# Kernel optimization log

Hardware: AMD Instinct MI355X
Metric: run time of the kernel (lower is better)

## Reference

```python
import jax, jax.numpy as jnp
import numpy as np

NUM_NODES = 100000
EMBED_DIM = 128
HIDDEN_DIM = 128
NUM_EDGES = 600000
NUM_LABELS = 200000


def setup_inputs() -> dict:
    key = jax.random.key(0)
    ks = jax.random.split(key, 12)
    edge_index = jax.random.randint(ks[0], (2, NUM_EDGES), 0, NUM_NODES)
    edge_label_index = jax.random.randint(ks[1], (2, NUM_LABELS), 0, NUM_NODES)
    s = 0.05
    return {
        "edge_index": edge_index,
        "edge_label_index": edge_label_index,
        "emb": jax.random.normal(ks[2], (NUM_NODES, EMBED_DIM), jnp.float32) * s,
        # conv1: lin_l (aggregated neighbors, with bias), lin_r (root, no bias)
        "W1l": jax.random.normal(ks[3], (EMBED_DIM, HIDDEN_DIM), jnp.float32) * s,
        "b1": jnp.zeros((HIDDEN_DIM,), jnp.float32),
        "W1r": jax.random.normal(ks[4], (EMBED_DIM, HIDDEN_DIM), jnp.float32) * s,
        # conv2
        "W2l": jax.random.normal(ks[5], (HIDDEN_DIM, HIDDEN_DIM), jnp.float32) * s,
        "b2": jnp.zeros((HIDDEN_DIM,), jnp.float32),
        "W2r": jax.random.normal(ks[6], (HIDDEN_DIM, HIDDEN_DIM), jnp.float32) * s,
        # final link predictor Linear(2*hidden, 1)
        "Wlin": jax.random.normal(ks[7], (2 * HIDDEN_DIM, 1), jnp.float32) * s,
        "blin": jnp.zeros((1,), jnp.float32),
    }


def _sage_conv(x, src, dst, Wl, bl, Wr):
    # mean aggregation of source-node features at destination nodes
    n = x.shape[0]
    msg_sum = jax.ops.segment_sum(x[src], dst, num_segments=n)  # [N, d]
    cnt = jax.ops.segment_sum(jnp.ones_like(src, dtype=x.dtype), dst, num_segments=n)
    agg = msg_sum / jnp.maximum(cnt, 1.0)[:, None]
    return agg @ Wl + bl + x @ Wr


def reference(edge_index, edge_label_index, emb, W1l, b1, W1r, W2l, b2, W2r, Wlin, blin):
    src, dst = edge_index[0], edge_index[1]
    x = jax.nn.relu(_sage_conv(emb, src, dst, W1l, b1, W1r))
    x = _sage_conv(x, src, dst, W2l, b2, W2r)
    s, d = edge_label_index[0], edge_label_index[1]
    pair = jnp.concatenate([x[s], x[d]], axis=1)  # [L, 2*hidden]
    return (pair @ Wlin + blin).reshape(-1)
```

## Files before the change

kernel.cpp:

```cpp
#include <hip/hip_runtime.h>
#include <hip/hip_bf16.h>

#define N_NODES 100000
#define N_EDGES 600000
#define N_LABELS 200000
#define DIM 128
#define NPARTS 391
#define MT 64
#define NMT 1563
#define FG_GRID 768
#define LDA 136
#define LDC 280

using short8 = __attribute__((ext_vector_type(8))) short;
using f32x2  = __attribute__((ext_vector_type(2))) float;
using f32x4  = __attribute__((ext_vector_type(4))) float;
using u32x2  = __attribute__((ext_vector_type(2))) unsigned;
using u32x4  = __attribute__((ext_vector_type(4))) unsigned;

__device__ __forceinline__ float b2f(short s) {
    union { unsigned u; float f; } c;
    c.u = ((unsigned)(unsigned short)s) << 16;
    return c.f;
}
__device__ __forceinline__ f32x2 b2f2(unsigned u) {
    union { unsigned u; float f; } lo, hi;
    lo.u = u << 16;
    hi.u = u & 0xffff0000u;
    f32x2 r; r[0] = lo.f; r[1] = hi.f;
    return r;
}
__device__ __forceinline__ short f2b(float f) {
    __hip_bfloat16 h = __float2bfloat16(f);
    return *reinterpret_cast<short*>(&h);
}
__device__ __forceinline__ unsigned f2b2u(float x, float y) {
    __hip_bfloat162 h = __float22bfloat162_rn(make_float2(x, y));
    return *reinterpret_cast<unsigned*>(&h);
}

__global__ void prep_k(const float* __restrict__ W1l, const float* __restrict__ W1r,
                       short* __restrict__ BT1,
                       const float* __restrict__ W2l, const float* __restrict__ W2r,
                       const float* __restrict__ Wlin, const float* __restrict__ b2,
                       float* __restrict__ up, float* __restrict__ uq,
                       float* __restrict__ vp, float* __restrict__ vq,
                       float2* __restrict__ cpq, int* __restrict__ cnt) {
    int b = blockIdx.x;
    int t = threadIdx.x;
    if (b < 128) {
        int i = b * 256 + t;
        int n = i >> 7, k = i & 127;
        float v = (n < 128) ? W1l[k * 128 + n] : W1r[k * 128 + (n - 128)];
        BT1[n * 128 + k] = f2b(v);
    } else if (b == 128) {
        const float* W = (t < 128) ? W2l : W2r;
        int k = t & 127;
        float s0 = 0.f, s1 = 0.f;
        for (int n = 0; n < 128; ++n) {
            float w = W[k * 128 + n];
            s0 += w * Wlin[n];
            s1 += w * Wlin[128 + n];
        }
        if (t < 128) { up[k] = s0; uq[k] = s1; }
        else         { vp[k] = s0; vq[k] = s1; }
    } else if (b == 129) {
        if (t < 64) {
            float p0 = b2[t] * Wlin[t] + b2[t + 64] * Wlin[t + 64];
            float q0 = b2[t] * Wlin[128 + t] + b2[t + 64] * Wlin[192 + t];
#pragma unroll
            for (int m = 1; m <= 32; m <<= 1) {
                p0 += __shfl_xor(p0, m, 64);
                q0 += __shfl_xor(q0, m, 64);
            }
            if (t == 0) *cpq = make_float2(p0, q0);
        }
    } else {
        int i = (b - 130) * 256 + t;
        if (i < N_NODES) cnt[i] = 0;
    }
}

__global__ void count_k(const int* __restrict__ ei, int* __restrict__ cnt,
                        int* __restrict__ rank) {
    int e = blockIdx.x * blockDim.x + threadIdx.x;
    if (e < N_EDGES) rank[e] = atomicAdd(&cnt[ei[N_EDGES + e]], 1);
}

__global__ void scan1_k(const int* __restrict__ cnt, int* __restrict__ rowptr,
                        int* __restrict__ partials) {
    __shared__ int s[256];
    int t = threadIdx.x;
    int i = blockIdx.x * 256 + t;
    int v = (i < N_NODES) ? cnt[i] : 0;
    s[t] = v;
    __syncthreads();
    for (int off = 1; off < 256; off <<= 1) {
        int x = s[t];
        int y = (t >= off) ? s[t - off] : 0;
        __syncthreads();
        s[t] = x + y;
        __syncthreads();
    }
    if (i < N_NODES) rowptr[i] = s[t] - v;
    if (t == 255) partials[blockIdx.x] = s[255];
}

__global__ void scanB_k(const int* __restrict__ partials, int* __restrict__ rowptr) {
    __shared__ int s[512];
    __shared__ int base_s;
    int t = threadIdx.x;
    int v = (t < NPARTS) ? partials[t] : 0;
    s[t] = v;
    __syncthreads();
    for (int off = 1; off < 512; off <<= 1) {
        int x = s[t];
        int y = (t >= off) ? s[t - off] : 0;
        __syncthreads();
        s[t] = x + y;
        __syncthreads();
    }
    int b = blockIdx.x;
    if (t == 0) base_s = (b > 0) ? s[b - 1] : 0;
    if (b == 0 && t == 0) rowptr[N_NODES] = s[NPARTS - 1];
    __syncthreads();
    if (t < 256) {
        int i = b * 256 + t;
        if (i < N_NODES) rowptr[i] += base_s;
    }
}

__global__ __launch_bounds__(256, 3) void fillgemm_k(const int* __restrict__ ei,
                                                     const int* __restrict__ rank,
                                                     const int* __restrict__ rowptr,
                                                     int* __restrict__ adj,
                                                     const float* __restrict__ Af,
                                                     const short* __restrict__ BT,
                                                     short* __restrict__ Hl,
                                                     short* __restrict__ Hr) {
    __shared__ short lA[MT * LDA];
    __shared__ short lC[MT * LDC];
    int tid = threadIdx.x;

    for (int e = blockIdx.x * 256 + tid; e < N_EDGES; e += FG_GRID * 256) {
        int d = ei[N_EDGES + e];
        adj[rowptr[d] + rank[e]] = ei[e];
    }

    int lane = tid & 63;
    int wave = tid >> 6;
    int quad = lane >> 4;
    int l16  = lane & 15;

    short8 Wf[4][4];
#pragma unroll
    for (int t = 0; t < 4; ++t)
#pragma unroll
        for (int kk = 0; kk < 4; ++kk)
            Wf[t][kk] = *(const short8*)(BT + (wave * 64 + t * 16 + l16) * DIM + kk * 32 + quad * 8);

    for (int mt = blockIdx.x; mt < NMT; mt += FG_GRID) {
        long base = (long)mt * MT;

        __syncthreads();
#pragma unroll
        for (int i = 0; i < 8; ++i) {
            int c = tid + i * 256;
            int row = c >> 5;
            int k4 = (c & 31) << 2;
            long grow = base + row;
            f32x4 a;
            if (grow < N_NODES) a = *(const f32x4*)(Af + grow * DIM + k4);
            else { a[0] = 0.f; a[1] = 0.f; a[2] = 0.f; a[3] = 0.f; }
            u32x2 o;
            o[0] = f2b2u(a[0], a[1]);
            o[1] = f2b2u(a[2], a[3]);
            *(u32x2*)(lA + row * LDA + k4) = o;
        }
        __syncthreads();

#pragma unroll
        for (int sub = 0; sub < 4; ++sub) {
            int r0 = sub * 16;
            short8 xf[4];
#pragma unroll
            for (int kk = 0; kk < 4; ++kk)
                xf[kk] = *(const short8*)(lA + (r0 + l16) * LDA + kk * 32 + quad * 8);
            f32x4 acc[4];
#pragma unroll
            for (int t = 0; t < 4; ++t)
#pragma unroll
                for (int r = 0; r < 4; ++r) acc[t][r] = 0.f;
#pragma unroll
            for (int kk = 0; kk < 4; ++kk)
#pragma unroll
                for (int t = 0; t < 4; ++t)
                    acc[t] = __builtin_amdgcn_mfma_f32_16x16x32_bf16(Wf[t][kk], xf[kk], acc[t], 0, 0, 0);
#pragma unroll
            for (int t = 0; t < 4; ++t) {
                u32x2 o;
                o[0] = f2b2u(acc[t][0], acc[t][1]);
                o[1] = f2b2u(acc[t][2], acc[t][3]);
                *(u32x2*)(lC + (r0 + l16) * LDC + wave * 64 + t * 16 + quad * 4) = o;
            }
        }
        __syncthreads();

#pragma unroll
        for (int half = 0; half < 2; ++half) {
            short* __restrict__ H = half ? Hr : Hl;
#pragma unroll
            for (int i = 0; i < 4; ++i) {
                int c2 = tid + i * 256;
                int row = c2 >> 4;
                int f8 = (c2 & 15) << 3;
                long grow = base + row;
                if (grow < N_NODES) {
                    short8 v = *(const short8*)(lC + row * LDC + half * 128 + f8);
                    *(short8*)(H + grow * DIM + f8) = v;
                }
            }
        }
    }
}

__device__ __forceinline__ void gather_mean(const short* __restrict__ Hl,
                                            const int* __restrict__ rowptr,
                                            const int* __restrict__ adj,
                                            int node, int lane, f32x2 sum[4], float& inv) {
    int g  = lane >> 4;
    int f0 = (lane & 15) << 3;
    int beg = rowptr[node];
    int deg = rowptr[node + 1] - beg;
#pragma unroll
    for (int d = 0; d < 4; ++d) { sum[d][0] = 0.f; sum[d][1] = 0.f; }

    int av = (lane < deg) ? adj[beg + lane] : 0;
    int degc = deg < 64 ? deg : 64;

    u32x4 h0;
    bool v0 = false;
    if (degc > 0) {
        int idx = __shfl(av, g, 64);
        v0 = g < degc;
        if (v0) h0 = *(const u32x4*)(Hl + (long)idx * DIM + f0);
    }
    for (int e0 = 4; e0 < degc; e0 += 4) {
        int idx = __shfl(av, e0 + g, 64);
        bool v1 = (e0 + g) < degc;
        u32x4 h1;
        if (v1) h1 = *(const u32x4*)(Hl + (long)idx * DIM + f0);
        if (v0) {
#pragma unroll
            for (int d = 0; d < 4; ++d) sum[d] += b2f2(h0[d]);
        }
        h0 = h1; v0 = v1;
    }
    if (v0) {
#pragma unroll
        for (int d = 0; d < 4; ++d) sum[d] += b2f2(h0[d]);
    }
    for (int e0 = 64; e0 < deg; e0 += 4) {
        int e = e0 + g;
        if (e < deg) {
            int idx = adj[beg + e];
            u32x4 h = *(const u32x4*)(Hl + (long)idx * DIM + f0);
#pragma unroll
            for (int d = 0; d < 4; ++d) sum[d] += b2f2(h[d]);
        }
    }
#pragma unroll
    for (int d = 0; d < 4; ++d)
#pragma unroll
        for (int c = 0; c < 2; ++c) {
            sum[d][c] += __shfl_xor(sum[d][c], 16, 64);
            sum[d][c] += __shfl_xor(sum[d][c], 32, 64);
        }
    inv = deg > 0 ? 1.f / (float)deg : 0.f;
}

__global__ void agg1_k(const short* __restrict__ Hl, const short* __restrict__ Hr,
                       const int* __restrict__ rowptr, const int* __restrict__ adj,
                       const float* __restrict__ b1,
                       const float* __restrict__ up, const float* __restrict__ uq,
                       const float* __restrict__ vp, const float* __restrict__ vq,
                       float2* __restrict__ S, float2* __restrict__ T) {
    int lane = threadIdx.x & 63;
    int node = blockIdx.x * 4 + (threadIdx.x >> 6);
    int f0 = (lane & 15) << 3;
    if (node >= N_NODES) return;

    f32x2 sum[4]; float inv;
    gather_mean(Hl, rowptr, adj, node, lane, sum, inv);

    u32x4 hru = *(const u32x4*)(Hr + (long)node * DIM + f0);
    f32x2 x2[4];
#pragma unroll
    for (int d = 0; d < 4; ++d) {
        f32x2 hr2 = b2f2(hru[d]);
        f32x2 bb  = *(const f32x2*)(b1 + f0 + 2 * d);
        f32x2 v   = sum[d] * inv + hr2 + bb;
        x2[d][0] = fmaxf(v[0], 0.f);
        x2[d][1] = fmaxf(v[1], 0.f);
    }

    f32x2 ap2 = {0.f, 0.f}, aq2 = {0.f, 0.f}, tp2 = {0.f, 0.f}, tq2 = {0.f, 0.f};
#pragma unroll
    for (int d = 0; d < 4; ++d) {
        f32x2 u0 = *(const f32x2*)(up + f0 + 2 * d);
        f32x2 u1 = *(const f32x2*)(uq + f0 + 2 * d);
        f32x2 w0 = *(const f32x2*)(vp + f0 + 2 * d);
        f32x2 w1 = *(const f32x2*)(vq + f0 + 2 * d);
        ap2 += x2[d] * u0;
        aq2 += x2[d] * u1;
        tp2 += x2[d] * w0;
        tq2 += x2[d] * w1;
    }
    float ap = ap2[0] + ap2[1], aq = aq2[0] + aq2[1];
    float tp = tp2[0] + tp2[1], tq = tq2[0] + tq2[1];
#pragma unroll
    for (int m = 1; m <= 8; m <<= 1) {
        ap += __shfl_xor(ap, m, 64);
        aq += __shfl_xor(aq, m, 64);
        tp += __shfl_xor(tp, m, 64);
        tq += __shfl_xor(tq, m, 64);
    }
    if (lane == 0) {
        S[node] = make_float2(ap, aq);
        T[node] = make_float2(tp, tq);
    }
}

__global__ void agg2_k(const int* __restrict__ rowptr, const int* __restrict__ adj,
                       const float2* __restrict__ S, const float2* __restrict__ T,
                       const float2* __restrict__ cpq,
                       float* __restrict__ p, float* __restrict__ q) {
    int lane = threadIdx.x & 63;
    int wavei = blockIdx.x * 4 + (threadIdx.x >> 6);
    int slot = lane & 3;
    int node = wavei * 16 + (lane >> 2);
    if (node >= N_NODES) return;
    int beg = rowptr[node], end = rowptr[node + 1];
    float sp = 0.f, sq = 0.f;
    for (int e = beg + slot; e < end; e += 4) {
        float2 v = S[adj[e]];
        sp += v.x; sq += v.y;
    }
    sp += __shfl_xor(sp, 1, 64); sp += __shfl_xor(sp, 2, 64);
    sq += __shfl_xor(sq, 1, 64); sq += __shfl_xor(sq, 2, 64);
    if (slot == 0) {
        int deg = end - beg;
        float inv = deg > 0 ? 1.f / (float)deg : 0.f;
        float2 t = T[node];
        float2 c = *cpq;
        p[node] = sp * inv + t.x + c.x;
        q[node] = sq * inv + t.y + c.y;
    }
}

__global__ void out_k(const int* __restrict__ eli, const float* __restrict__ p,
                      const float* __restrict__ q, const float* __restrict__ blin,
                      float* __restrict__ out) {
    int i = blockIdx.x * blockDim.x + threadIdx.x;
    if (i < N_LABELS) out[i] = p[eli[i]] + q[eli[N_LABELS + i]] + blin[0];
}


extern "C" void kernel_launch(void* const* d_in, const int* in_sizes, int n_in,
                              void* d_out, int out_size, void* d_ws, size_t ws_size,
                              hipStream_t stream) {
    const int*   edge_index = (const int*)d_in[0];
    const int*   eli        = (const int*)d_in[1];
    const float* emb        = (const float*)d_in[2];
    const float* W1l        = (const float*)d_in[3];
    const float* b1         = (const float*)d_in[4];
    const float* W1r        = (const float*)d_in[5];
    const float* W2l        = (const float*)d_in[6];
    const float* b2         = (const float*)d_in[7];
    const float* W2r        = (const float*)d_in[8];
    const float* Wlin       = (const float*)d_in[9];
    const float* blin       = (const float*)d_in[10];
    float* out = (float*)d_out;

    char* ws = (char*)d_ws;
    size_t off = 0;
    auto alloc = [&](size_t bytes) -> void* {
        off = (off + 255) & ~(size_t)255;
        void* ptr = ws + off;
        off += bytes;
        return ptr;
    };

    short* Hl  = (short*)alloc((size_t)N_NODES * DIM * 2);
    short* Hr  = (short*)alloc((size_t)N_NODES * DIM * 2);
    short* BT1 = (short*)alloc(256 * 128 * 2);
    float* up = (float*)alloc(128 * 4);
    float* uq = (float*)alloc(128 * 4);
    float* vp = (float*)alloc(128 * 4);
    float* vq = (float*)alloc(128 * 4);
    float2* cpq = (float2*)alloc(8);
    int* cnt      = (int*)alloc((size_t)N_NODES * 4);
    int* rowptr   = (int*)alloc((size_t)(N_NODES + 1) * 4);
    int* rank     = (int*)alloc((size_t)N_EDGES * 4);
    int* adj      = (int*)alloc((size_t)N_EDGES * 4);
    int* partials = (int*)alloc(NPARTS * 4);
    float2* S     = (float2*)alloc((size_t)N_NODES * 8);
    float2* T     = (float2*)alloc((size_t)N_NODES * 8);
    float* p      = (float*)alloc((size_t)N_NODES * 4);
    float* q      = (float*)alloc((size_t)N_NODES * 4);

    prep_k<<<130 + NPARTS, 256, 0, stream>>>(W1l, W1r, BT1, W2l, W2r, Wlin, b2,
                                             up, uq, vp, vq, cpq, cnt);
    count_k<<<(N_EDGES + 255) / 256, 256, 0, stream>>>(edge_index, cnt, rank);
    scan1_k<<<NPARTS, 256, 0, stream>>>(cnt, rowptr, partials);
    scanB_k<<<NPARTS, 512, 0, stream>>>(partials, rowptr);

    fillgemm_k<<<FG_GRID, 256, 0, stream>>>(edge_index, rank, rowptr, adj, emb, BT1, Hl, Hr);

    agg1_k<<<N_NODES / 4, 256, 0, stream>>>(Hl, Hr, rowptr, adj, b1, up, uq, vp, vq, S, T);

    agg2_k<<<(N_NODES + 63) / 64, 256, 0, stream>>>(rowptr, adj, S, T, cpq, p, q);
    out_k<<<(N_LABELS + 255) / 256, 256, 0, stream>>>(eli, p, q, blin, out);
}
```

Measured before the change: 233.2 us.

## Map four nodes per wavefront in agg1 and fuse edge counting into prep

The layer-1 aggregation kernel now gives each node a 16-lane group instead of a whole 64-lane wavefront. Neighbors are walked serially within the group, which removes the cross-group shuffle reductions and the idle lanes on low-degree nodes. Separately, the count-zeroing moves to hipMemsetAsync, and the edge-degree atomic counting is merged into the prep kernel, saving one kernel launch. The trade-off is that each lane now loads neighbors one at a time, which lengthens the dependent chain for high-degree nodes.

```diff
diff --git a/kernel.cpp b/kernel.cpp
--- a/kernel.cpp
+++ b/kernel.cpp
@@ -11,6 +11,7 @@
 #define FG_GRID 768
 #define LDA 136
 #define LDC 280
+#define CNT_BLOCKS 2344
 
 using short8 = __attribute__((ext_vector_type(8))) short;
 using f32x2  = __attribute__((ext_vector_type(2))) float;
@@ -45,7 +46,9 @@
                        const float* __restrict__ Wlin, const float* __restrict__ b2,
                        float* __restrict__ up, float* __restrict__ uq,
                        float* __restrict__ vp, float* __restrict__ vq,
-                       float2* __restrict__ cpq, int* __restrict__ cnt) {
+                       float2* __restrict__ cpq,
+                       const int* __restrict__ ei, int* __restrict__ cnt,
+                       int* __restrict__ rank) {
     int b = blockIdx.x;
     int t = threadIdx.x;
     if (b < 128) {
@@ -76,15 +79,9 @@
             if (t == 0) *cpq = make_float2(p0, q0);
         }
     } else {
-        int i = (b - 130) * 256 + t;
-        if (i < N_NODES) cnt[i] = 0;
-    }
-}
-
-__global__ void count_k(const int* __restrict__ ei, int* __restrict__ cnt,
-                        int* __restrict__ rank) {
-    int e = blockIdx.x * blockDim.x + threadIdx.x;
-    if (e < N_EDGES) rank[e] = atomicAdd(&cnt[ei[N_EDGES + e]], 1);
+        int e = (b - 130) * 256 + t;
+        if (e < N_EDGES) rank[e] = atomicAdd(&cnt[ei[N_EDGES + e]], 1);
+    }
 }
 
 __global__ void scan1_k(const int* __restrict__ cnt, int* __restrict__ rowptr,
@@ -224,74 +221,54 @@
     }
 }
 
-__device__ __forceinline__ void gather_mean(const short* __restrict__ Hl,
-                                            const int* __restrict__ rowptr,
-                                            const int* __restrict__ adj,
-                                            int node, int lane, f32x2 sum[4], float& inv) {
-    int g  = lane >> 4;
-    int f0 = (lane & 15) << 3;
-    int beg = rowptr[node];
-    int deg = rowptr[node + 1] - beg;
-#pragma unroll
-    for (int d = 0; d < 4; ++d) { sum[d][0] = 0.f; sum[d][1] = 0.f; }
-
-    int av = (lane < deg) ? adj[beg + lane] : 0;
-    int degc = deg < 64 ? deg : 64;
-
-    u32x4 h0;
-    bool v0 = false;
-    if (degc > 0) {
-        int idx = __shfl(av, g, 64);
-        v0 = g < degc;
-        if (v0) h0 = *(const u32x4*)(Hl + (long)idx * DIM + f0);
-    }
-    for (int e0 = 4; e0 < degc; e0 += 4) {
-        int idx = __shfl(av, e0 + g, 64);
-        bool v1 = (e0 + g) < degc;
-        u32x4 h1;
-        if (v1) h1 = *(const u32x4*)(Hl + (long)idx * DIM + f0);
-        if (v0) {
-#pragma unroll
-            for (int d = 0; d < 4; ++d) sum[d] += b2f2(h0[d]);
-        }
-        h0 = h1; v0 = v1;
-    }
-    if (v0) {
-#pragma unroll
-        for (int d = 0; d < 4; ++d) sum[d] += b2f2(h0[d]);
-    }
-    for (int e0 = 64; e0 < deg; e0 += 4) {
-        int e = e0 + g;
-        if (e < deg) {
-            int idx = adj[beg + e];
-            u32x4 h = *(const u32x4*)(Hl + (long)idx * DIM + f0);
-#pragma unroll
-            for (int d = 0; d < 4; ++d) sum[d] += b2f2(h[d]);
-        }
-    }
-#pragma unroll
-    for (int d = 0; d < 4; ++d)
-#pragma unroll
-        for (int c = 0; c < 2; ++c) {
-            sum[d][c] += __shfl_xor(sum[d][c], 16, 64);
-            sum[d][c] += __shfl_xor(sum[d][c], 32, 64);
-        }
-    inv = deg > 0 ? 1.f / (float)deg : 0.f;
-}
-
 __global__ void agg1_k(const short* __restrict__ Hl, const short* __restrict__ Hr,
                        const int* __restrict__ rowptr, const int* __restrict__ adj,
                        const float* __restrict__ b1,
                        const float* __restrict__ up, const float* __restrict__ uq,
                        const float* __restrict__ vp, const float* __restrict__ vq,
                        float2* __restrict__ S, float2* __restrict__ T) {
-    int lane = threadIdx.x & 63;
-    int node = blockIdx.x * 4 + (threadIdx.x >> 6);
-    int f0 = (lane & 15) << 3;
-    if (node >= N_NODES) return;
-
-    f32x2 sum[4]; float inv;
-    gather_mean(Hl, rowptr, adj, node, lane, sum, inv);
+    int lane  = threadIdx.x & 63;
+    int wavei = blockIdx.x * 4 + (threadIdx.x >> 6);
+    int g   = lane >> 4;
+    int l16 = lane & 15;
+    int f0  = l16 << 3;
+    int node = wavei * 4 + g;
+
+    int beg = rowptr[node];
+    int deg = rowptr[node + 1] - beg;
+
+    int av = (l16 < deg) ? adj[beg + l16] : 0;
+    int degc = deg < 16 ? deg : 16;
+
+    f32x2 sum[4];
+#pragma unroll
+    for (int d = 0; d < 4; ++d) { sum[d][0] = 0.f; sum[d][1] = 0.f; }
+
+    u32x4 h0;
+    bool v0 = (degc > 0);
+    if (v0) {
+        int idx = __shfl(av, (g << 4), 64);
+        h0 = *(const u32x4*)(Hl + (long)idx * DIM + f0);
+    }
+    for (int j = 1; j < degc; ++j) {
+        int idx = __shfl(av, (g << 4) + j, 64);
+        u32x4 h1 = *(const u32x4*)(Hl + (long)idx * DIM + f0);
+#pragma unroll
+        for (int d = 0; d < 4; ++d) sum[d] += b2f2(h0[d]);
+        h0 = h1;
+    }
+    if (v0) {
+#pragma unroll
+        for (int d = 0; d < 4; ++d) sum[d] += b2f2(h0[d]);
+    }
+    for (int e = beg + 16; e < beg + deg; ++e) {
+        int idx = adj[e];
+        u32x4 h = *(const u32x4*)(Hl + (long)idx * DIM + f0);
+#pragma unroll
+        for (int d = 0; d < 4; ++d) sum[d] += b2f2(h[d]);
+    }
+
+    float inv = deg > 0 ? 1.f / (float)deg : 0.f;
 
     u32x4 hru = *(const u32x4*)(Hr + (long)node * DIM + f0);
     f32x2 x2[4];
@@ -325,7 +302,7 @@
         tp += __shfl_xor(tp, m, 64);
         tq += __shfl_xor(tq, m, 64);
     }
-    if (lane == 0) {
+    if (l16 == 0) {
         S[node] = make_float2(ap, aq);
         T[node] = make_float2(tp, tq);
     }
@@ -409,15 +386,16 @@
     float* p      = (float*)alloc((size_t)N_NODES * 4);
     float* q      = (float*)alloc((size_t)N_NODES * 4);
 
-    prep_k<<<130 + NPARTS, 256, 0, stream>>>(W1l, W1r, BT1, W2l, W2r, Wlin, b2,
-                                             up, uq, vp, vq, cpq, cnt);
-    count_k<<<(N_EDGES + 255) / 256, 256, 0, stream>>>(edge_index, cnt, rank);
+    hipMemsetAsync(cnt, 0, (size_t)N_NODES * 4, stream);
+    prep_k<<<130 + CNT_BLOCKS, 256, 0, stream>>>(W1l, W1r, BT1, W2l, W2r, Wlin, b2,
+                                                 up, uq, vp, vq, cpq,
+                                                 edge_index, cnt, rank);
     scan1_k<<<NPARTS, 256, 0, stream>>>(cnt, rowptr, partials);
     scanB_k<<<NPARTS, 512, 0, stream>>>(partials, rowptr);
 
     fillgemm_k<<<FG_GRID, 256, 0, stream>>>(edge_index, rank, rowptr, adj, emb, BT1, Hl, Hr);
 
-    agg1_k<<<N_NODES / 4, 256, 0, stream>>>(Hl, Hr, rowptr, adj, b1, up, uq, vp, vq, S, T);
+    agg1_k<<<N_NODES / 16, 256, 0, stream>>>(Hl, Hr, rowptr, adj, b1, up, uq, vp, vq, S, T);
 
     agg2_k<<<(N_NODES + 63) / 64, 256, 0, stream>>>(rowptr, adj, S, T, cpq, p, q);
     out_k<<<(N_LABELS + 255) / 256, 256, 0, stream>>>(eli, p, q, blin, out);
```

Result: faster. 207.8 us (-10.9%).
